# Performance work log

Hardware: AMD Instinct MI355X
Metric: run time of the kernel (lower is better)

The kernel has to match this reference:

```python
import jax, jax.numpy as jnp
import numpy as np
import math

N_HEADS = 16
D_EMBED = 1024
D_HEAD = D_EMBED // N_HEADS
SEQ_LEN = 4096
N_GRAPHS = 16


def setup_inputs() -> dict:
    key = jax.random.key(0)
    ks = jax.random.split(key, 6)
    x = jax.random.normal(ks[0], (SEQ_LEN, D_EMBED), dtype=jnp.float32)
    batch = jnp.sort(jax.random.randint(ks[1], (SEQ_LEN,), 0, N_GRAPHS, dtype=jnp.int64))
    s_in = 1.0 / math.sqrt(D_EMBED)
    W_in = jax.random.normal(ks[2], (D_EMBED, 3 * D_EMBED), dtype=jnp.float32) * s_in
    b_in = jnp.zeros((3 * D_EMBED,), dtype=jnp.float32)
    W_out = jax.random.normal(ks[3], (D_EMBED, D_EMBED), dtype=jnp.float32) * s_in
    b_out = jnp.zeros((D_EMBED,), dtype=jnp.float32)
    return {"x": x, "batch": batch, "W_in": W_in, "b_in": b_in, "W_out": W_out, "b_out": b_out}


def reference(x, batch, W_in, b_in, W_out, b_out):
    # x: [N, D]; batch: [N] graph ids
    n, d = x.shape
    qkv = x @ W_in + b_in                      # [N, 3D]
    q, k, v = jnp.split(qkv, 3, axis=-1)
    # [N, H, dh] -> [H, N, dh]
    q = q.reshape(n, N_HEADS, D_HEAD).transpose(1, 0, 2)
    k = k.reshape(n, N_HEADS, D_HEAD).transpose(1, 0, 2)
    v = v.reshape(n, N_HEADS, D_HEAD).transpose(1, 0, 2)
    weight = jnp.einsum('hnd,hmd->hnm', q, k)  # [H, N, N]
    # Faithful to original: in-block mask value is 1.0 (not 0), out-of-block -inf,
    # added BEFORE dividing by sqrt(d_head).
    same = batch[:, None] == batch[None, :]
    mask = jnp.where(same, 1.0, -jnp.inf).astype(weight.dtype)
    weight = (weight + mask) / math.sqrt(D_HEAD)
    weight = jax.nn.softmax(weight, axis=-1)
    out = jnp.einsum('hnm,hmd->hnd', weight, v)  # [H, N, dh]
    out = out.transpose(1, 0, 2).reshape(n, d)
    return out @ W_out + b_out
```

## Files before the change

kernel.cpp:

```cpp
#include <hip/hip_runtime.h>
#include <math.h>

#define NT 4096
#define DE 1024
#define NH 16
#define DH 64
#define NG 16

typedef unsigned short u16;
typedef __attribute__((ext_vector_type(8))) short short8;
typedef __attribute__((ext_vector_type(4))) float f32x4;

__device__ __forceinline__ u16 f2bf(float f) {
    unsigned u = __float_as_uint(f);
    unsigned r = (u + 0x7FFF + ((u >> 16) & 1)) >> 16;
    return (u16)r;
}
__device__ __forceinline__ u16 f2bf_trunc(float f) {
    return (u16)(__float_as_uint(f) >> 16);
}

__device__ __forceinline__ void gld_lds16(const u16* g, u16* l) {
    __builtin_amdgcn_global_load_lds(
        (const __attribute__((address_space(1))) unsigned int*)g,
        (__attribute__((address_space(3))) unsigned int*)l, 16, 0, 0);
}

__global__ __launch_bounds__(256) void prep_k(
        const float* __restrict__ x, u16* __restrict__ xb,
        const int* __restrict__ batch, int* __restrict__ bounds,
        const float* __restrict__ W_in, u16* __restrict__ Wt_in,
        const float* __restrict__ W_out, u16* __restrict__ Wt_out) {
    __shared__ float Ls[32][33];
    int bid = blockIdx.x;
    int t = threadIdx.x;
    if (bid < 4096) {
        if (bid == 0 && t <= NG) {
            int g = t, lo = 0, hi = NT;
            while (lo < hi) {
                int mid = (lo + hi) >> 1;
                if (batch[mid] < g) lo = mid + 1;
                else hi = mid;
            }
            bounds[g] = lo;
        }
        int i = bid * 256 + t;
        float4 v = *(const float4*)(x + (size_t)i * 4);
        ushort4 o = make_ushort4(f2bf(v.x), f2bf(v.y), f2bf(v.z), f2bf(v.w));
        *(ushort4*)(xb + (size_t)i * 4) = o;
        return;
    }
    int tb = bid - 4096;
    const float* W; u16* Wt; int N, k0, n0;
    if (tb < 3072) { W = W_in;  Wt = Wt_in;  N = 3 * DE; k0 = (tb & 31) * 32; n0 = (tb >> 5) * 32; }
    else { tb -= 3072; W = W_out; Wt = Wt_out; N = DE;   k0 = (tb & 31) * 32; n0 = (tb >> 5) * 32; }
    int row = t >> 3;
    int c4  = (t & 7) * 4;
    float4 v = *(const float4*)(W + (size_t)(k0 + row) * N + n0 + c4);
    Ls[row][c4 + 0] = v.x; Ls[row][c4 + 1] = v.y;
    Ls[row][c4 + 2] = v.z; Ls[row][c4 + 3] = v.w;
    __syncthreads();
    ushort4 o = make_ushort4(f2bf(Ls[c4 + 0][row]), f2bf(Ls[c4 + 1][row]),
                             f2bf(Ls[c4 + 2][row]), f2bf(Ls[c4 + 3][row]));
    *(ushort4*)(Wt + (size_t)(n0 + row) * DE + k0 + c4) = o;
}

template<int FM, int FN, typename OutT>
__global__ __launch_bounds__(256) void gemm_mfma_bt(
        const u16* __restrict__ A, const u16* __restrict__ Bt,
        const float* __restrict__ bias, OutT* __restrict__ C,
        int M, int N, int K) {
    __shared__ u16 As[32 * FM * 64];
    __shared__ u16 Bs[32 * FN * 64];
    const int tid  = threadIdx.x;
    const int wave = tid >> 6;
    const int lane = tid & 63;
    const int l15  = lane & 15;
    const int quad = lane >> 4;
    const int m0 = blockIdx.y * 32 * FM;
    const int n0 = blockIdx.x * 32 * FN;
    const int wm = (wave >> 1) * 16 * FM;
    const int wn = (wave & 1) * 16 * FN;

    f32x4 acc[FM][FN];
#pragma unroll
    for (int i = 0; i < FM; ++i)
#pragma unroll
        for (int j = 0; j < FN; ++j) acc[i][j] = (f32x4){0.f, 0.f, 0.f, 0.f};

    const int srow = lane >> 3;
    const int scol = ((lane & 7) ^ srow) * 8;
    const int xq   = l15 & 7;

    for (int k0 = 0; k0 < K; k0 += 64) {
#pragma unroll
        for (int s = wave; s < 4 * FM; s += 4)
            gld_lds16(A + (size_t)(m0 + s * 8 + srow) * K + k0 + scol, &As[s * 512]);
#pragma unroll
        for (int s = wave; s < 4 * FN; s += 4)
            gld_lds16(Bt + (size_t)(n0 + s * 8 + srow) * K + k0 + scol, &Bs[s * 512]);
        __syncthreads();

#pragma unroll
        for (int kh = 0; kh < 2; ++kh) {
            const int xb_ = 4 * kh + quad;
            short8 af[FM], bf[FN];
#pragma unroll
            for (int it = 0; it < FM; ++it)
                af[it] = *(const short8*)&As[(wm + 16 * it + l15) * 64 + ((xb_ ^ xq) * 8)];
#pragma unroll
            for (int jt = 0; jt < FN; ++jt)
                bf[jt] = *(const short8*)&Bs[(wn + 16 * jt + l15) * 64 + ((xb_ ^ xq) * 8)];
#pragma unroll
            for (int it = 0; it < FM; ++it)
#pragma unroll
                for (int jt = 0; jt < FN; ++jt)
                    acc[it][jt] = __builtin_amdgcn_mfma_f32_16x16x32_bf16(
                        af[it], bf[jt], acc[it][jt], 0, 0, 0);
        }
        __syncthreads();
    }

#pragma unroll
    for (int jt = 0; jt < FN; ++jt) {
        int col = n0 + wn + 16 * jt + l15;
        float bv = bias[col];
#pragma unroll
        for (int it = 0; it < FM; ++it) {
            int rbase = m0 + wm + 16 * it + quad * 4;
#pragma unroll
            for (int r = 0; r < 4; ++r) {
                float v = acc[it][jt][r] + bv;
                if constexpr (sizeof(OutT) == 2)
                    C[(size_t)(rbase + r) * N + col] = (OutT)f2bf(v);
                else
                    C[(size_t)(rbase + r) * N + col] = v;
            }
        }
    }
}

__global__ __launch_bounds__(256) void attn_mfma_k(
        const u16* __restrict__ qkv, const int* __restrict__ bounds,
        u16* __restrict__ out) {
    const int h  = blockIdx.x;
    const int g  = blockIdx.y;
    const int qt = blockIdx.z;
    const int s0 = bounds[g];
    const int s1 = bounds[g + 1];
    const int q0 = s0 + qt * 128;
    if (q0 >= s1) return;
    const int nq = min(128, s1 - q0);

    __shared__ u16 Ks[2][64 * 64];
    __shared__ u16 Vt[2][64][72];
    __shared__ u16 Ps[64][72];

    const int tid  = threadIdx.x;
    const int wave = tid >> 6;
    const int lane = tid & 63;
    const int l15  = lane & 15;
    const int quad = lane >> 4;

    short8 qf[2][2];
#pragma unroll
    for (int qs = 0; qs < 2; ++qs) {
        int qrow = qs * 64 + wave * 16 + l15;
        uint4 a = {0, 0, 0, 0}, b = {0, 0, 0, 0};
        if (qrow < nq) {
            const u16* src = qkv + (size_t)(q0 + qrow) * 3072 + h * 64 + quad * 8;
            a = *(const uint4*)src;
            b = *(const uint4*)(src + 32);
        }
        qf[qs][0] = *(short8*)&a;
        qf[qs][1] = *(short8*)&b;
    }

    short8 onesf;
#pragma unroll
    for (int j = 0; j < 8; ++j) onesf[j] = (short)0x3F80;

    f32x4 o_acc[2][4];
    f32x4 l_acc[2];
#pragma unroll
    for (int qs = 0; qs < 2; ++qs) {
        l_acc[qs] = (f32x4){0.f, 0.f, 0.f, 0.f};
#pragma unroll
        for (int ct = 0; ct < 4; ++ct) o_acc[qs][ct] = (f32x4){0.f, 0.f, 0.f, 0.f};
    }

    const int nIter = (s1 - s0 + 63) >> 6;
    const int srow = lane >> 3;
    const int scol = ((lane & 7) ^ srow) * 8;

    auto stageK = [&](int it2, int buf) {
#pragma unroll
        for (int i = 0; i < 2; ++i) {
            int s = wave + 4 * i;
            gld_lds16(qkv + (size_t)(s0 + it2 * 64 + s * 8 + srow) * 3072 + 1024 + h * 64 + scol,
                      &Ks[buf][s * 512]);
        }
    };
    auto stageV = [&](int it2, int buf) {
        int r0 = 2 * (tid & 31);
        int c0 = (tid >> 5) * 8;
        const u16* src = qkv + (size_t)(s0 + it2 * 64 + r0) * 3072 + 2048 + h * 64 + c0;
        uint4 a = *(const uint4*)src;
        uint4 b = *(const uint4*)(src + 3072);
        const u16* pa = (const u16*)&a;
        const u16* pb = (const u16*)&b;
#pragma unroll
        for (int j = 0; j < 8; ++j) {
            unsigned w = (unsigned)pa[j] | ((unsigned)pb[j] << 16);
            *(unsigned*)&Vt[buf][c0 + j][r0] = w;
        }
    };

    stageK(0, 0);
    stageV(0, 0);
    __syncthreads();

    const float CEXP = 0.125f * 1.44269504f;
    const int xq = l15 & 7;

    for (int it = 0; it < nIter; ++it) {
        const int k0 = s0 + it * 64;
        const int buf = it & 1;
        if (it + 1 < nIter) { stageK(it + 1, buf ^ 1); stageV(it + 1, buf ^ 1); }

        const bool fullTile = (k0 + 64 <= s1);

#pragma unroll
        for (int qs = 0; qs < 2; ++qs) {
            f32x4 s[4];
#pragma unroll
            for (int ct = 0; ct < 4; ++ct) {
                int row = ct * 16 + l15;
                short8 kf0 = *(const short8*)&Ks[buf][row * 64 + ((quad ^ xq) * 8)];
                short8 kf1 = *(const short8*)&Ks[buf][row * 64 + (((4 + quad) ^ xq) * 8)];
                f32x4 acc = (f32x4){0.f, 0.f, 0.f, 0.f};
                acc = __builtin_amdgcn_mfma_f32_16x16x32_bf16(qf[qs][0], kf0, acc, 0, 0, 0);
                acc = __builtin_amdgcn_mfma_f32_16x16x32_bf16(qf[qs][1], kf1, acc, 0, 0, 0);
                s[ct] = acc;
            }

            if (fullTile) {
#pragma unroll
                for (int ct = 0; ct < 4; ++ct)
#pragma unroll
                    for (int r = 0; r < 4; ++r)
                        Ps[wave * 16 + quad * 4 + r][ct * 16 + l15] =
                            f2bf_trunc(exp2f(s[ct][r] * CEXP));
            } else {
#pragma unroll
                for (int ct = 0; ct < 4; ++ct) {
                    bool valid = (k0 + ct * 16 + l15) < s1;
#pragma unroll
                    for (int r = 0; r < 4; ++r)
                        Ps[wave * 16 + quad * 4 + r][ct * 16 + l15] =
                            valid ? f2bf_trunc(exp2f(s[ct][r] * CEXP)) : (u16)0;
                }
            }

            short8 pf0 = *(const short8*)&Ps[wave * 16 + l15][quad * 8];
            short8 pf1 = *(const short8*)&Ps[wave * 16 + l15][quad * 8 + 32];

            l_acc[qs] = __builtin_amdgcn_mfma_f32_16x16x32_bf16(pf0, onesf, l_acc[qs], 0, 0, 0);
            l_acc[qs] = __builtin_amdgcn_mfma_f32_16x16x32_bf16(pf1, onesf, l_acc[qs], 0, 0, 0);
#pragma unroll
            for (int ct = 0; ct < 4; ++ct) {
                short8 vf0 = *(const short8*)&Vt[buf][ct * 16 + l15][quad * 8];
                short8 vf1 = *(const short8*)&Vt[buf][ct * 16 + l15][quad * 8 + 32];
                o_acc[qs][ct] = __builtin_amdgcn_mfma_f32_16x16x32_bf16(pf0, vf0, o_acc[qs][ct], 0, 0, 0);
                o_acc[qs][ct] = __builtin_amdgcn_mfma_f32_16x16x32_bf16(pf1, vf1, o_acc[qs][ct], 0, 0, 0);
            }
        }
        __syncthreads();
    }

#pragma unroll
    for (int qs = 0; qs < 2; ++qs)
#pragma unroll
        for (int r = 0; r < 4; ++r) {
            int row = qs * 64 + wave * 16 + quad * 4 + r;
            if (row < nq) {
                float inv = 1.f / l_acc[qs][r];
#pragma unroll
                for (int ct = 0; ct < 4; ++ct)
                    out[(size_t)(q0 + row) * 1024 + h * 64 + ct * 16 + l15] =
                        f2bf(o_acc[qs][ct][r] * inv);
            }
        }
}

extern "C" void kernel_launch(void* const* d_in, const int* in_sizes, int n_in,
                              void* d_out, int out_size, void* d_ws, size_t ws_size,
                              hipStream_t stream) {
    const float* x     = (const float*)d_in[0];
    const int*   batch = (const int*)d_in[1];
    const float* W_in  = (const float*)d_in[2];
    const float* b_in  = (const float*)d_in[3];
    const float* W_out = (const float*)d_in[4];
    const float* b_out = (const float*)d_in[5];
    float* out = (float*)d_out;

    u16* qkvb   = (u16*)d_ws;
    u16* attnb  = qkvb + (size_t)NT * 3 * DE;
    u16* xb     = attnb + (size_t)NT * DE;
    u16* Wt_in  = xb + (size_t)NT * DE;
    u16* Wt_out = Wt_in + (size_t)3 * DE * DE;
    int* bounds = (int*)(Wt_out + (size_t)DE * DE);

    prep_k<<<8192, 256, 0, stream>>>(x, xb, batch, bounds, W_in, Wt_in, W_out, Wt_out);

    gemm_mfma_bt<4, 4, u16><<<dim3(3 * DE / 128, NT / 128), 256, 0, stream>>>(
        xb, Wt_in, b_in, qkvb, NT, 3 * DE, DE);

    attn_mfma_k<<<dim3(NH, NG, 4), 256, 0, stream>>>(qkvb, bounds, attnb);

    gemm_mfma_bt<2, 4, float><<<dim3(DE / 128, NT / 64), 256, 0, stream>>>(
        attnb, Wt_out, b_out, out, NT, DE, DE);
}
```

Measured before the change: 152.0 us.

## Double-buffer GEMM LDS tiles and stage bf16 epilogue through shared memory

The GEMM main loop now uses two LDS buffers per operand and issues the global-to-LDS loads for the next K tile before computing on the current one, so memory latency overlaps with MFMA work and one barrier per iteration is dropped. The bf16 output path now writes accumulators into an LDS tile and then emits coalesced 16-byte row stores instead of scattered 2-byte stores. The cost is double the LDS footprint, which may lower occupancy. The epilogue is hardcoded to FN==4 through a static_assert.

```diff
diff --git a/kernel.cpp b/kernel.cpp
--- a/kernel.cpp
+++ b/kernel.cpp
@@ -70,8 +70,8 @@
         const u16* __restrict__ A, const u16* __restrict__ Bt,
         const float* __restrict__ bias, OutT* __restrict__ C,
         int M, int N, int K) {
-    __shared__ u16 As[32 * FM * 64];
-    __shared__ u16 Bs[32 * FN * 64];
+    __shared__ u16 As[2][32 * FM * 64];
+    __shared__ u16 Bs[2][32 * FN * 64];
     const int tid  = threadIdx.x;
     const int wave = tid >> 6;
     const int lane = tid & 63;
@@ -92,49 +92,85 @@
     const int scol = ((lane & 7) ^ srow) * 8;
     const int xq   = l15 & 7;
 
-    for (int k0 = 0; k0 < K; k0 += 64) {
+    auto stage = [&](int kt, int buf) {
 #pragma unroll
         for (int s = wave; s < 4 * FM; s += 4)
-            gld_lds16(A + (size_t)(m0 + s * 8 + srow) * K + k0 + scol, &As[s * 512]);
+            gld_lds16(A + (size_t)(m0 + s * 8 + srow) * K + kt * 64 + scol, &As[buf][s * 512]);
 #pragma unroll
         for (int s = wave; s < 4 * FN; s += 4)
-            gld_lds16(Bt + (size_t)(n0 + s * 8 + srow) * K + k0 + scol, &Bs[s * 512]);
-        __syncthreads();
+            gld_lds16(Bt + (size_t)(n0 + s * 8 + srow) * K + kt * 64 + scol, &Bs[buf][s * 512]);
+    };
+
+    const int nIter = K >> 6;
+    stage(0, 0);
+    __syncthreads();
+
+    for (int it = 0; it < nIter; ++it) {
+        const int buf = it & 1;
+        if (it + 1 < nIter) stage(it + 1, buf ^ 1);
 
 #pragma unroll
         for (int kh = 0; kh < 2; ++kh) {
             const int xb_ = 4 * kh + quad;
             short8 af[FM], bf[FN];
 #pragma unroll
-            for (int it = 0; it < FM; ++it)
-                af[it] = *(const short8*)&As[(wm + 16 * it + l15) * 64 + ((xb_ ^ xq) * 8)];
-#pragma unroll
-            for (int jt = 0; jt < FN; ++jt)
-                bf[jt] = *(const short8*)&Bs[(wn + 16 * jt + l15) * 64 + ((xb_ ^ xq) * 8)];
-#pragma unroll
-            for (int it = 0; it < FM; ++it)
-#pragma unroll
-                for (int jt = 0; jt < FN; ++jt)
-                    acc[it][jt] = __builtin_amdgcn_mfma_f32_16x16x32_bf16(
-                        af[it], bf[jt], acc[it][jt], 0, 0, 0);
+            for (int i2 = 0; i2 < FM; ++i2)
+                af[i2] = *(const short8*)&As[buf][(wm + 16 * i2 + l15) * 64 + ((xb_ ^ xq) * 8)];
+#pragma unroll
+            for (int j2 = 0; j2 < FN; ++j2)
+                bf[j2] = *(const short8*)&Bs[buf][(wn + 16 * j2 + l15) * 64 + ((xb_ ^ xq) * 8)];
+#pragma unroll
+            for (int i2 = 0; i2 < FM; ++i2)
+#pragma unroll
+                for (int j2 = 0; j2 < FN; ++j2)
+                    acc[i2][j2] = __builtin_amdgcn_mfma_f32_16x16x32_bf16(
+                        af[i2], bf[j2], acc[i2][j2], 0, 0, 0);
         }
         __syncthreads();
     }
 
-#pragma unroll
-    for (int jt = 0; jt < FN; ++jt) {
-        int col = n0 + wn + 16 * jt + l15;
-        float bv = bias[col];
-#pragma unroll
-        for (int it = 0; it < FM; ++it) {
-            int rbase = m0 + wm + 16 * it + quad * 4;
-#pragma unroll
-            for (int r = 0; r < 4; ++r) {
-                float v = acc[it][jt][r] + bv;
-                if constexpr (sizeof(OutT) == 2)
-                    C[(size_t)(rbase + r) * N + col] = (OutT)f2bf(v);
-                else
-                    C[(size_t)(rbase + r) * N + col] = v;
+    if constexpr (sizeof(OutT) == 2) {
+        static_assert(FN == 4, "bf16 epilogue assumes BN=128");
+        u16 (*Cs)[136] = (u16(*)[136]) & As[0][0];
+#pragma unroll
+        for (int ro = 0; ro < (32 * FM) / 64; ++ro) {
+            int rbase = wm - ro * 64;
+            if (rbase >= 0 && rbase < 64) {
+#pragma unroll
+                for (int jt = 0; jt < FN; ++jt) {
+                    int col = wn + 16 * jt + l15;
+                    float bv = bias[n0 + col];
+#pragma unroll
+                    for (int i2 = 0; i2 < FM; ++i2) {
+                        if (16 * i2 >= 64) break;
+#pragma unroll
+                        for (int r = 0; r < 4; ++r)
+                            Cs[rbase + 16 * i2 + quad * 4 + r][col] =
+                                f2bf(acc[i2][jt][r] + bv);
+                    }
+                }
+            }
+            __syncthreads();
+#pragma unroll
+            for (int i2 = 0; i2 < 4; ++i2) {
+                int row = i2 * 16 + (tid >> 4);
+                int cc  = (tid & 15) * 8;
+                uint4 v = *(const uint4*)&Cs[row][cc];
+                *(uint4*)(C + (size_t)(m0 + ro * 64 + row) * N + n0 + cc) = v;
+            }
+            __syncthreads();
+        }
+    } else {
+#pragma unroll
+        for (int jt = 0; jt < FN; ++jt) {
+            int col = n0 + wn + 16 * jt + l15;
+            float bv = bias[col];
+#pragma unroll
+            for (int i2 = 0; i2 < FM; ++i2) {
+                int rbase = m0 + wm + 16 * i2 + quad * 4;
+#pragma unroll
+                for (int r = 0; r < 4; ++r)
+                    C[(size_t)(rbase + r) * N + col] = acc[i2][jt][r] + bv;
             }
         }
     }
```

Result: slower. 165.9 us (+9.2%).
